# Optimization experiments

Measured on AMD Instinct MI355X. Metric: run time of the kernel, lower is better.

## Reference

```python
import jax, jax.numpy as jnp
import numpy as np

N, D = 8192, 256
TEMP = 0.07


def setup_inputs() -> dict:
    key = jax.random.key(0)
    kx, ky = jax.random.split(key)
    x = jax.random.normal(kx, (N, D), dtype=jnp.float32)
    y = jax.random.normal(ky, (N, D), dtype=jnp.float32)
    # L2-normalize (standard for InfoNCE; keeps exp(sim/temp) finite)
    x = x / jnp.linalg.norm(x, axis=-1, keepdims=True)
    y = y / jnp.linalg.norm(y, axis=-1, keepdims=True)
    return {"x": x, "y": y}


def reference(x, y):
    # sim_matrix = exp(x @ y^T / temperature), shape [N, N]
    sim = jnp.exp(jnp.matmul(x, y.T) / TEMP)
    # positives: exp(<x_i, y_i>/T) == diagonal of sim
    l_pos = jnp.exp(jnp.sum(x * y, axis=-1) / TEMP)
    # negatives: row-sum excluding the diagonal (equivalent to masked_select)
    l_neg = jnp.sum(sim, axis=-1) - jnp.diagonal(sim)
    loss = jnp.mean(-jnp.log(l_pos / l_neg))
    return loss
```

## Files before the change

### kernel.cpp

```cpp
#include <hip/hip_runtime.h>
#include <hip/hip_bf16.h>

#define N_ROWS 8192
#define D_DIM  256

static constexpr float kQuantScale = 64.0f;
static constexpr float kScaleAcc = 20.609929155556627f / 4096.0f;
static constexpr float kInvTAcc  = 14.285714285714286f / 4096.0f;

typedef float f32x4 __attribute__((ext_vector_type(4)));
typedef long  lx2   __attribute__((ext_vector_type(2)));

__device__ __forceinline__ void gl_lds16(const void* g, void* l) {
  __builtin_amdgcn_global_load_lds(
      (const __attribute__((address_space(1))) void*)g,
      (__attribute__((address_space(3))) void*)l, 16, 0, 0);
}

__global__ __launch_bounds__(256)
void cvt_fp8_kernel(const float* __restrict__ x, const float* __restrict__ y,
                    unsigned char* __restrict__ xq, unsigned char* __restrict__ yq,
                    float* __restrict__ rowsum, unsigned int* __restrict__ done) {
  if (blockIdx.x == 0) {
    for (int i = threadIdx.x; i < N_ROWS; i += 256) rowsum[i] = 0.f;
    if (threadIdx.x == 0) *done = 0u;
  }
  const int per_mat = N_ROWS * D_DIM / 8;
  int idx = blockIdx.x * blockDim.x + threadIdx.x;
  const float* src = x;
  unsigned char* dst = xq;
  int i = idx;
  if (idx >= per_mat) { src = y; dst = yq; i = idx - per_mat; }
  float4 a = ((const float4*)src)[2 * (size_t)i];
  float4 b = ((const float4*)src)[2 * (size_t)i + 1];
  int v0 = 0, v1 = 0;
  v0 = __builtin_amdgcn_cvt_pk_fp8_f32(a.x * kQuantScale, a.y * kQuantScale, v0, false);
  v0 = __builtin_amdgcn_cvt_pk_fp8_f32(a.z * kQuantScale, a.w * kQuantScale, v0, true);
  v1 = __builtin_amdgcn_cvt_pk_fp8_f32(b.x * kQuantScale, b.y * kQuantScale, v1, false);
  v1 = __builtin_amdgcn_cvt_pk_fp8_f32(b.z * kQuantScale, b.w * kQuantScale, v1, true);
  const int row = i >> 5;
  const int c   = i & 31;
  const int ks  = c >> 2;
  const int q   = c & 3;
  const size_t off = (size_t)row * D_DIM + (ks >> 1) * 64 + q * 16 + (ks & 1) * 8;
  *(int2*)(dst + off) = make_int2(v0, v1);
}

__global__ __launch_bounds__(512, 1)
void infonce_gemm(const unsigned char* __restrict__ X,
                  const unsigned char* __restrict__ Y,
                  float* __restrict__ rowsum, float* __restrict__ diag,
                  unsigned int* __restrict__ done, float* __restrict__ out) {
  __shared__ unsigned char Xs[256 * 256];
  __shared__ unsigned char Ys[2][128 * 256];
  __shared__ unsigned int ticket_s;

  const int b  = blockIdx.x;
  const int bi = b >> 3;
  const int gj = b & 7;

  const int t    = threadIdx.x;
  const int lane = t & 63;
  const int wave = t >> 6;
  const int wm   = wave >> 1;
  const int wn   = wave & 1;
  const int quad = lane >> 4;
  const int l15  = lane & 15;

  const unsigned char* Xblk = X + (size_t)(bi * 256) * D_DIM;

#pragma unroll
  for (int it = 0; it < 8; ++it) {
    const int c0  = (it * 8 + wave) * 64;
    const int s   = c0 + lane;
    const int row = s >> 4;
    const int cg  = (s & 15) ^ (row & 15);
    gl_lds16(Xblk + (size_t)row * D_DIM + cg * 16, &Xs[c0 * 16]);
  }
  {
    const unsigned char* Yblk = Y + (size_t)(gj * 8) * 128 * D_DIM;
#pragma unroll
    for (int it = 0; it < 4; ++it) {
      const int c0  = (it * 8 + wave) * 64;
      const int s   = c0 + lane;
      const int row = s >> 4;
      const int cg  = (s & 15) ^ (row & 15);
      gl_lds16(Yblk + (size_t)row * D_DIM + cg * 16, &Ys[0][c0 * 16]);
    }
  }

  f32x4 acc[4][4];
#pragma unroll
  for (int a = 0; a < 4; ++a)
#pragma unroll
    for (int c = 0; c < 4; ++c) acc[a][c] = (f32x4){0.f, 0.f, 0.f, 0.f};

  for (int tt = 0; tt < 8; ++tt) {
    const int p = tt & 1;

    __syncthreads();

    if (tt < 7) {
      const unsigned char* Yblk = Y + (size_t)(gj * 8 + tt + 1) * 128 * D_DIM;
#pragma unroll
      for (int it = 0; it < 4; ++it) {
        const int c0  = (it * 8 + wave) * 64;
        const int s   = c0 + lane;
        const int row = s >> 4;
        const int cg  = (s & 15) ^ (row & 15);
        gl_lds16(Yblk + (size_t)row * D_DIM + cg * 16, &Ys[p ^ 1][c0 * 16]);
      }
    }

#pragma unroll
    for (int g = 0; g < 4; ++g) {
      lx2 af[4], bfr[4];
#pragma unroll
      for (int mt = 0; mt < 4; ++mt) {
        const int row = wm * 64 + mt * 16 + l15;
        const int pos = (g * 4 + quad) ^ l15;
        af[mt] = *(const lx2*)(&Xs[row * 256 + pos * 16]);
      }
#pragma unroll
      for (int nt = 0; nt < 4; ++nt) {
        const int row = wn * 64 + nt * 16 + l15;
        const int pos = (g * 4 + quad) ^ l15;
        bfr[nt] = *(const lx2*)(&Ys[p][row * 256 + pos * 16]);
      }
#pragma unroll
      for (int sub = 0; sub < 2; ++sub)
#pragma unroll
        for (int mt = 0; mt < 4; ++mt)
#pragma unroll
          for (int nt = 0; nt < 4; ++nt)
            acc[mt][nt] = __builtin_amdgcn_mfma_f32_16x16x32_fp8_fp8(
                af[mt][sub], bfr[nt][sub], acc[mt][nt], 0, 0, 0);
    }

    const int gi_base = bi * 256 + wm * 64;
#pragma unroll
    for (int mt = 0; mt < 4; ++mt) {
#pragma unroll
      for (int rr = 0; rr < 4; ++rr) {
        float part = 0.f;
#pragma unroll
        for (int nt = 0; nt < 4; ++nt)
          part += __builtin_amdgcn_exp2f(acc[mt][nt][rr] * kScaleAcc);
        part += __shfl_xor(part, 1);
        part += __shfl_xor(part, 2);
        part += __shfl_xor(part, 4);
        part += __shfl_xor(part, 8);
        if (l15 == 0) atomicAdd(&rowsum[gi_base + mt * 16 + quad * 4 + rr], part);
      }
    }
    {
      const int ct = gj * 8 + tt;
      const bool d0 = (ct == 2 * bi)     && (wm == wn);
      const bool d1 = (ct == 2 * bi + 1) && (wm == wn + 2);
      if (d0 || d1) {
#pragma unroll
        for (int nt = 0; nt < 4; ++nt)
#pragma unroll
          for (int rr = 0; rr < 4; ++rr)
            if (l15 == quad * 4 + rr)
              atomicExch(&diag[gi_base + nt * 16 + l15], acc[nt][nt][rr]);
      }
    }
#pragma unroll
    for (int a = 0; a < 4; ++a)
#pragma unroll
      for (int c = 0; c < 4; ++c) acc[a][c] = (f32x4){0.f, 0.f, 0.f, 0.f};
  }

  __syncthreads();
  if (t == 0) ticket_s = atomicAdd(done, 1u);
  __syncthreads();
  if (ticket_s == 255u) {
    __threadfence();
    float local = 0.f;
    for (int i = t; i < N_ROWS; i += 512) {
      const float rs = atomicAdd(&rowsum[i], 0.0f);
      const float d  = atomicAdd(&diag[i], 0.0f);
      local += __logf(rs - __builtin_amdgcn_exp2f(d * kScaleAcc)) - d * kInvTAcc;
    }
    float* red = (float*)Xs;
    red[t] = local;
    __syncthreads();
    for (int s2 = 256; s2 > 0; s2 >>= 1) {
      if (t < s2) red[t] += red[t + s2];
      __syncthreads();
    }
    if (t == 0) out[0] = red[0] / (float)N_ROWS;
  }
}

extern "C" void kernel_launch(void* const* d_in, const int* in_sizes, int n_in,
                              void* d_out, int out_size, void* d_ws, size_t ws_size,
                              hipStream_t stream) {
  const float* x = (const float*)d_in[0];
  const float* y = (const float*)d_in[1];
  float* out = (float*)d_out;

  float* rowsum = (float*)d_ws;
  float* diag   = rowsum + N_ROWS;
  unsigned int* done = (unsigned int*)(diag + N_ROWS);
  unsigned char* xq = (unsigned char*)d_ws + 2 * N_ROWS * sizeof(float) + 16;
  unsigned char* yq = xq + (size_t)N_ROWS * D_DIM;

  int cvt_blocks = 2 * N_ROWS * D_DIM / 8 / 256;
  cvt_fp8_kernel<<<cvt_blocks, 256, 0, stream>>>(x, y, xq, yq, rowsum, done);

  infonce_gemm<<<256, 512, 0, stream>>>(xq, yq, rowsum, diag, done, out);
}
```

Measured before the change: 118.8 us.

## Pre-swizzle fp8 operands into MFMA fragment layout and load directly to registers

The conversion kernel now writes X and Y in a fragment-major layout that matches the MFMA operand order, so each wave can load its operands with coalesced 16-byte global loads straight into registers. The GEMM drops LDS staging and barriers entirely. Each wave keeps one 64-column Y strip resident in registers and streams eight 64-row X bands from global/L2. The grid becomes 512 blocks of 256 threads with two blocks per CU. The risk is that X is no longer shared across waves through LDS, so global/L2 traffic rises and load latency is exposed without explicit double buffering.

After: 184.3 us. 55.1% more time.

```diff
diff --git a/kernel.cpp b/kernel.cpp
--- a/kernel.cpp
+++ b/kernel.cpp
@@ -11,15 +11,9 @@
 typedef float f32x4 __attribute__((ext_vector_type(4)));
 typedef long  lx2   __attribute__((ext_vector_type(2)));
 
-__device__ __forceinline__ void gl_lds16(const void* g, void* l) {
-  __builtin_amdgcn_global_load_lds(
-      (const __attribute__((address_space(1))) void*)g,
-      (__attribute__((address_space(3))) void*)l, 16, 0, 0);
-}
-
 __global__ __launch_bounds__(256)
 void cvt_fp8_kernel(const float* __restrict__ x, const float* __restrict__ y,
-                    unsigned char* __restrict__ xq, unsigned char* __restrict__ yq,
+                    unsigned char* __restrict__ xf, unsigned char* __restrict__ yf,
                     float* __restrict__ rowsum, unsigned int* __restrict__ done) {
   if (blockIdx.x == 0) {
     for (int i = threadIdx.x; i < N_ROWS; i += 256) rowsum[i] = 0.f;
@@ -28,9 +22,9 @@
   const int per_mat = N_ROWS * D_DIM / 8;
   int idx = blockIdx.x * blockDim.x + threadIdx.x;
   const float* src = x;
-  unsigned char* dst = xq;
+  unsigned char* dst = xf;
   int i = idx;
-  if (idx >= per_mat) { src = y; dst = yq; i = idx - per_mat; }
+  if (idx >= per_mat) { src = y; dst = yf; i = idx - per_mat; }
   float4 a = ((const float4*)src)[2 * (size_t)i];
   float4 b = ((const float4*)src)[2 * (size_t)i + 1];
   int v0 = 0, v1 = 0;
@@ -40,53 +34,40 @@
   v1 = __builtin_amdgcn_cvt_pk_fp8_f32(b.z * kQuantScale, b.w * kQuantScale, v1, true);
   const int row = i >> 5;
   const int c   = i & 31;
-  const int ks  = c >> 2;
   const int q   = c & 3;
-  const size_t off = (size_t)row * D_DIM + (ks >> 1) * 64 + q * 16 + (ks & 1) * 8;
+  const int sub = (c >> 2) & 1;
+  const int g   = c >> 3;
+  const int mt  = (row >> 4) & 3;
+  const int l15 = row & 15;
+  const int band = row >> 6;
+  const size_t off = (size_t)band * 16384 + (mt * 4 + g) * 1024
+                   + (q * 16 + l15) * 16 + sub * 8;
   *(int2*)(dst + off) = make_int2(v0, v1);
 }
 
-__global__ __launch_bounds__(512, 1)
-void infonce_gemm(const unsigned char* __restrict__ X,
-                  const unsigned char* __restrict__ Y,
+__global__ __launch_bounds__(256, 2)
+void infonce_gemm(const unsigned char* __restrict__ Xf,
+                  const unsigned char* __restrict__ Yf,
                   float* __restrict__ rowsum, float* __restrict__ diag,
                   unsigned int* __restrict__ done, float* __restrict__ out) {
-  __shared__ unsigned char Xs[256 * 256];
-  __shared__ unsigned char Ys[2][128 * 256];
+  __shared__ float red[256];
   __shared__ unsigned int ticket_s;
 
-  const int b  = blockIdx.x;
-  const int bi = b >> 3;
-  const int gj = b & 7;
-
+  const int b    = blockIdx.x;
+  const int seg  = b >> 5;
+  const int sq   = b & 31;
   const int t    = threadIdx.x;
   const int lane = t & 63;
   const int wave = t >> 6;
-  const int wm   = wave >> 1;
-  const int wn   = wave & 1;
+  const int strip = sq * 4 + wave;
   const int quad = lane >> 4;
   const int l15  = lane & 15;
 
-  const unsigned char* Xblk = X + (size_t)(bi * 256) * D_DIM;
-
+  lx2 yreg[16];
+  {
+    const lx2* Yb = (const lx2*)(Yf + (size_t)strip * 16384 + lane * 16);
 #pragma unroll
-  for (int it = 0; it < 8; ++it) {
-    const int c0  = (it * 8 + wave) * 64;
-    const int s   = c0 + lane;
-    const int row = s >> 4;
-    const int cg  = (s & 15) ^ (row & 15);
-    gl_lds16(Xblk + (size_t)row * D_DIM + cg * 16, &Xs[c0 * 16]);
-  }
-  {
-    const unsigned char* Yblk = Y + (size_t)(gj * 8) * 128 * D_DIM;
-#pragma unroll
-    for (int it = 0; it < 4; ++it) {
-      const int c0  = (it * 8 + wave) * 64;
-      const int s   = c0 + lane;
-      const int row = s >> 4;
-      const int cg  = (s & 15) ^ (row & 15);
-      gl_lds16(Yblk + (size_t)row * D_DIM + cg * 16, &Ys[0][c0 * 16]);
-    }
+    for (int i = 0; i < 16; ++i) yreg[i] = Yb[i * 64];
   }
 
   f32x4 acc[4][4];
@@ -95,38 +76,18 @@
 #pragma unroll
     for (int c = 0; c < 4; ++c) acc[a][c] = (f32x4){0.f, 0.f, 0.f, 0.f};
 
-  for (int tt = 0; tt < 8; ++tt) {
-    const int p = tt & 1;
+  for (int ch = 0; ch < 8; ++ch) {
+    const int band = seg * 8 + ch;
 
-    __syncthreads();
-
-    if (tt < 7) {
-      const unsigned char* Yblk = Y + (size_t)(gj * 8 + tt + 1) * 128 * D_DIM;
+    lx2 areg[16];
+    {
+      const lx2* Ab = (const lx2*)(Xf + (size_t)band * 16384 + lane * 16);
 #pragma unroll
-      for (int it = 0; it < 4; ++it) {
-        const int c0  = (it * 8 + wave) * 64;
-        const int s   = c0 + lane;
-        const int row = s >> 4;
-        const int cg  = (s & 15) ^ (row & 15);
-        gl_lds16(Yblk + (size_t)row * D_DIM + cg * 16, &Ys[p ^ 1][c0 * 16]);
-      }
+      for (int i = 0; i < 16; ++i) areg[i] = Ab[i * 64];
     }
 
 #pragma unroll
-    for (int g = 0; g < 4; ++g) {
-      lx2 af[4], bfr[4];
-#pragma unroll
-      for (int mt = 0; mt < 4; ++mt) {
-        const int row = wm * 64 + mt * 16 + l15;
-        const int pos = (g * 4 + quad) ^ l15;
-        af[mt] = *(const lx2*)(&Xs[row * 256 + pos * 16]);
-      }
-#pragma unroll
-      for (int nt = 0; nt < 4; ++nt) {
-        const int row = wn * 64 + nt * 16 + l15;
-        const int pos = (g * 4 + quad) ^ l15;
-        bfr[nt] = *(const lx2*)(&Ys[p][row * 256 + pos * 16]);
-      }
+    for (int g = 0; g < 4; ++g)
 #pragma unroll
       for (int sub = 0; sub < 2; ++sub)
 #pragma unroll
@@ -134,10 +95,9 @@
 #pragma unroll
           for (int nt = 0; nt < 4; ++nt)
             acc[mt][nt] = __builtin_amdgcn_mfma_f32_16x16x32_fp8_fp8(
-                af[mt][sub], bfr[nt][sub], acc[mt][nt], 0, 0, 0);
-    }
+                areg[mt * 4 + g][sub], yreg[nt * 4 + g][sub], acc[mt][nt], 0, 0, 0);
 
-    const int gi_base = bi * 256 + wm * 64;
+    const int gi_base = band * 64;
 #pragma unroll
     for (int mt = 0; mt < 4; ++mt) {
 #pragma unroll
@@ -153,18 +113,13 @@
         if (l15 == 0) atomicAdd(&rowsum[gi_base + mt * 16 + quad * 4 + rr], part);
       }
     }
-    {
-      const int ct = gj * 8 + tt;
-      const bool d0 = (ct == 2 * bi)     && (wm == wn);
-      const bool d1 = (ct == 2 * bi + 1) && (wm == wn + 2);
-      if (d0 || d1) {
+    if (strip == band) {
 #pragma unroll
-        for (int nt = 0; nt < 4; ++nt)
+      for (int nt = 0; nt < 4; ++nt)
 #pragma unroll
-          for (int rr = 0; rr < 4; ++rr)
-            if (l15 == quad * 4 + rr)
-              atomicExch(&diag[gi_base + nt * 16 + l15], acc[nt][nt][rr]);
-      }
+        for (int rr = 0; rr < 4; ++rr)
+          if (l15 == quad * 4 + rr)
+            atomicExch(&diag[gi_base + nt * 16 + l15], acc[nt][nt][rr]);
     }
 #pragma unroll
     for (int a = 0; a < 4; ++a)
@@ -175,18 +130,17 @@
   __syncthreads();
   if (t == 0) ticket_s = atomicAdd(done, 1u);
   __syncthreads();
-  if (ticket_s == 255u) {
+  if (ticket_s == 511u) {
     __threadfence();
     float local = 0.f;
-    for (int i = t; i < N_ROWS; i += 512) {
+    for (int i = t; i < N_ROWS; i += 256) {
       const float rs = atomicAdd(&rowsum[i], 0.0f);
       const float d  = atomicAdd(&diag[i], 0.0f);
       local += __logf(rs - __builtin_amdgcn_exp2f(d * kScaleAcc)) - d * kInvTAcc;
     }
-    float* red = (float*)Xs;
     red[t] = local;
     __syncthreads();
-    for (int s2 = 256; s2 > 0; s2 >>= 1) {
+    for (int s2 = 128; s2 > 0; s2 >>= 1) {
       if (t < s2) red[t] += red[t + s2];
       __syncthreads();
     }
@@ -204,11 +158,11 @@
   float* rowsum = (float*)d_ws;
   float* diag   = rowsum + N_ROWS;
   unsigned int* done = (unsigned int*)(diag + N_ROWS);
-  unsigned char* xq = (unsigned char*)d_ws + 2 * N_ROWS * sizeof(float) + 16;
-  unsigned char* yq = xq + (size_t)N_ROWS * D_DIM;
+  unsigned char* xf = (unsigned char*)d_ws + 2 * N_ROWS * sizeof(float) + 16;
+  unsigned char* yf = xf + (size_t)N_ROWS * D_DIM;
 
   int cvt_blocks = 2 * N_ROWS * D_DIM / 8 / 256;
-  cvt_fp8_kernel<<<cvt_blocks, 256, 0, stream>>>(x, y, xq, yq, rowsum, done);
+  cvt_fp8_kernel<<<cvt_blocks, 256, 0, stream>>>(x, y, xf, yf, rowsum, done);
 
-  infonce_gemm<<<256, 512, 0, stream>>>(xq, yq, rowsum, diag, done, out);
+  infonce_gemm<<<512, 256, 0, stream>>>(xf, yf, rowsum, diag, done, out);
 }
```
